# Kernel tuning notes

Measured on AMD Instinct MI355X. Metric: run time of the kernel, lower is better.

The kernel has to match this reference:

```python
import jax, jax.numpy as jnp
import numpy as np

B = 32768
L = 1024            # harmonics length (from 1365 = L + L//3)
HID = 256
OUT = 1024


def setup_inputs() -> dict:
    key = jax.random.key(0)
    k1, k2, k3 = jax.random.split(key, 3)
    x = jax.random.normal(k1, (B, 1, L), dtype=jnp.float32)
    W1 = jax.random.normal(k2, (HID, 1365), dtype=jnp.float32) * 0.02
    b1 = jnp.zeros((HID,), dtype=jnp.float32)
    W2 = jax.random.normal(k3, (OUT, HID), dtype=jnp.float32) * 0.02
    b2 = jnp.zeros((OUT,), dtype=jnp.float32)
    return {"x": x, "W1": W1, "b1": b1, "W2": W2, "b2": b2}


def reference(x, W1, b1, W2, b2):
    # backbone is identity; squeeze channel dim -> harmonics_pred [B, L]
    h = x[:, 0, :]
    # multi-scale average pooling (method='average'), vectorized over batch
    s1 = h                                               # scale 1: [B, 1024]
    s2 = h[:, : (L // 2) * 2].reshape(-1, L // 2, 2).mean(axis=-1)   # [B, 512]
    s3 = h[:, : (L // 3) * 3].reshape(-1, L // 3, 3).mean(axis=-1)   # [B, 341]
    m = L // 3                                           # min_len = 341
    summed = s1[:, :m] + s2[:, :m] + s3                  # [B, 341]
    feat = jnp.concatenate([h, summed], axis=1)          # [B, 1365]
    # fund_head MLP (dropout inactive in eval)
    hid = jax.nn.relu(feat @ W1.T + b1)                  # [B, 256]
    fund = hid @ W2.T + b2                               # [B, 1024]
    return fund[:, None, :], h
```

## Files before the change

kernel.cpp:

```cpp
#include <hip/hip_runtime.h>
#include <stdint.h>
#include <stddef.h>

typedef __attribute__((ext_vector_type(8))) short short8;
typedef __attribute__((ext_vector_type(4))) float floatx4;

#define MFMA_BF16(A, B, C) __builtin_amdgcn_mfma_f32_16x16x32_bf16((A), (B), (C), 0, 0, 0)

static constexpr int NB   = 32768;
static constexpr int LV   = 1024;
static constexpr int HIDV = 256;
static constexpr int OUTV = 1024;
static constexpr size_t HOFF = (size_t)NB * OUTV;

__device__ __forceinline__ short f2bf(float f) {
  union { float f; uint32_t u; } c; c.f = f;
  uint32_t u = c.u;
  u += 0x7fffu + ((u >> 16) & 1u);
  return (short)(u >> 16);
}

__global__ __launch_bounds__(256) void wprep(const float* __restrict__ W1,
                                             const float* __restrict__ W2,
                                             short* __restrict__ w1bf,
                                             short* __restrict__ w2bf) {
  int idx = blockIdx.x * 256 + threadIdx.x;
  if (idx < 256 * 1024) {
    int n = idx >> 10;
    int k = idx & 1023;
    const float* r = W1 + (size_t)n * 1365;
    float v = r[k];
    if (k < 341)  v += r[1024 + k];
    if (k < 682)  v += 0.5f * r[1024 + (k >> 1)];
    if (k < 1023) v += (1.f / 3.f) * r[1024 + k / 3];
    w1bf[idx] = f2bf(v);
  } else {
    int j = idx - 256 * 1024;
    w2bf[j] = f2bf(W2[j]);
  }
}

__global__ __launch_bounds__(512, 4) void gemm_fused(
    const float* __restrict__ x,
    const short* __restrict__ w1bf, const short* __restrict__ w2bf,
    const float* __restrict__ b1, const float* __restrict__ b2,
    float* __restrict__ out) {
  __shared__ __align__(16) short Abuf[2][64 * 72];
  __shared__ __align__(16) short Hbuf[64 * 264];

  const int tid  = threadIdx.x;
  const int wave = tid >> 6;
  const int lane = tid & 63;
  const int l15  = lane & 15;
  const int quad = lane >> 4;
  const int row0 = blockIdx.x * 64;

  const int srow = tid >> 3;
  const int sseg = tid & 7;

  float4 xa, xb;
  const floatx4 fzero = {0.f, 0.f, 0.f, 0.f};

  const float4* xrow = reinterpret_cast<const float4*>(x + (size_t)(row0 + srow) * LV);
  float4* hrow = reinterpret_cast<float4*>(out + HOFF + (size_t)(row0 + srow) * LV);

  auto loadA = [&](int ck) {
    xa = xrow[ck * 16 + 2 * sseg];
    xb = xrow[ck * 16 + 2 * sseg + 1];
  };
  auto writeA = [&](int buf) {
    short8 p;
    p[0] = f2bf(xa.x); p[1] = f2bf(xa.y); p[2] = f2bf(xa.z); p[3] = f2bf(xa.w);
    p[4] = f2bf(xb.x); p[5] = f2bf(xb.y); p[6] = f2bf(xb.z); p[7] = f2bf(xb.w);
    *reinterpret_cast<short8*>(&Abuf[buf][srow * 72 + sseg * 8]) = p;
  };
  auto storeH = [&](int ck) {
    hrow[ck * 16 + 2 * sseg]     = xa;
    hrow[ck * 16 + 2 * sseg + 1] = xb;
  };

  short8 Breg[4], Bnxt[4];
  auto loadB1 = [&](int ck, short8* dst) {
    #pragma unroll
    for (int ks = 0; ks < 2; ++ks)
      #pragma unroll
      for (int ns = 0; ns < 2; ++ns)
        dst[ks * 2 + ns] = *reinterpret_cast<const short8*>(
            w1bf + (size_t)(wave * 32 + ns * 16 + l15) * LV + ck * 64 + ks * 32 + quad * 8);
  };

  floatx4 acc1[4][2];
  #pragma unroll
  for (int ms = 0; ms < 4; ++ms)
    #pragma unroll
    for (int ns = 0; ns < 2; ++ns)
      acc1[ms][ns] = fzero;

  loadA(0);
  loadB1(0, Breg);

  #pragma unroll 1
  for (int ck = 0; ck < 16; ++ck) {
    const int buf = ck & 1;
    writeA(buf);
    asm volatile("s_waitcnt lgkmcnt(0)" ::: "memory");
    __builtin_amdgcn_s_barrier();
    asm volatile("" ::: "memory");
    storeH(ck);
    if (ck < 15) { loadA(ck + 1); loadB1(ck + 1, Bnxt); }
    #pragma unroll
    for (int ks = 0; ks < 2; ++ks) {
      short8 afr[4];
      #pragma unroll
      for (int ms = 0; ms < 4; ++ms)
        afr[ms] = *reinterpret_cast<const short8*>(
            &Abuf[buf][(ms * 16 + l15) * 72 + ks * 32 + quad * 8]);
      #pragma unroll
      for (int ms = 0; ms < 4; ++ms)
        #pragma unroll
        for (int ns = 0; ns < 2; ++ns)
          acc1[ms][ns] = MFMA_BF16(afr[ms], Breg[ks * 2 + ns], acc1[ms][ns]);
    }
    #pragma unroll
    for (int i = 0; i < 4; ++i) Breg[i] = Bnxt[i];
  }

  #pragma unroll
  for (int ms = 0; ms < 4; ++ms) {
    #pragma unroll
    for (int ns = 0; ns < 2; ++ns) {
      const int n = wave * 32 + ns * 16 + l15;
      const float bias = b1[n];
      #pragma unroll
      for (int r = 0; r < 4; ++r) {
        const int m = ms * 16 + quad * 4 + r;
        float v = acc1[ms][ns][r] + bias;
        Hbuf[m * 264 + n] = f2bf(v > 0.f ? v : 0.f);
      }
    }
  }
  asm volatile("s_waitcnt lgkmcnt(0)" ::: "memory");
  __builtin_amdgcn_s_barrier();
  asm volatile("" ::: "memory");

  short8 B2[2], B2n[2];
  auto loadB2 = [&](int q, int kc, short8* dst) {
    #pragma unroll
    for (int ns = 0; ns < 2; ++ns)
      dst[ns] = *reinterpret_cast<const short8*>(
          w2bf + (size_t)(q * 256 + wave * 32 + ns * 16 + l15) * HIDV + kc * 32 + quad * 8);
  };

  loadB2(0, 0, B2);
  #pragma unroll 1
  for (int q = 0; q < 4; ++q) {
    floatx4 acc2[4][2];
    #pragma unroll
    for (int ms = 0; ms < 4; ++ms)
      #pragma unroll
      for (int ns = 0; ns < 2; ++ns)
        acc2[ms][ns] = fzero;
    #pragma unroll 1
    for (int kc = 0; kc < 8; ++kc) {
      short8 afr[4];
      #pragma unroll
      for (int ms = 0; ms < 4; ++ms)
        afr[ms] = *reinterpret_cast<const short8*>(
            &Hbuf[(ms * 16 + l15) * 264 + kc * 32 + quad * 8]);
      const int t = q * 8 + kc + 1;
      if (t < 32) loadB2(t >> 3, t & 7, B2n);
      #pragma unroll
      for (int ms = 0; ms < 4; ++ms)
        #pragma unroll
        for (int ns = 0; ns < 2; ++ns)
          acc2[ms][ns] = MFMA_BF16(afr[ms], B2[ns], acc2[ms][ns]);
      #pragma unroll
      for (int i = 0; i < 2; ++i) B2[i] = B2n[i];
    }
    #pragma unroll
    for (int ms = 0; ms < 4; ++ms) {
      #pragma unroll
      for (int ns = 0; ns < 2; ++ns) {
        const int o = q * 256 + wave * 32 + ns * 16 + l15;
        const float bias = b2[o];
        #pragma unroll
        for (int r = 0; r < 4; ++r) {
          const int m = ms * 16 + quad * 4 + r;
          out[(size_t)(row0 + m) * OUTV + o] = acc2[ms][ns][r] + bias;
        }
      }
    }
  }
}

extern "C" void kernel_launch(void* const* d_in, const int* in_sizes, int n_in,
                              void* d_out, int out_size, void* d_ws, size_t ws_size,
                              hipStream_t stream) {
  const float* x  = (const float*)d_in[0];
  const float* W1 = (const float*)d_in[1];
  const float* b1 = (const float*)d_in[2];
  const float* W2 = (const float*)d_in[3];
  const float* b2 = (const float*)d_in[4];
  float* out = (float*)d_out;

  char* ws = (char*)d_ws;
  short* w1bf = (short*)(ws);
  short* w2bf = (short*)(ws + 524288);

  hipLaunchKernelGGL(wprep, dim3(2048), dim3(256), 0, stream, W1, W2, w1bf, w2bf);
  hipLaunchKernelGGL(gemm_fused, dim3(NB / 64), dim3(512), 0, stream,
                     x, w1bf, w2bf, b1, b2, out);
}
```

Baseline: 416.2 us.

## Prefetch x two chunks ahead and use nontemporal loads and stores

The A-tile load of x now runs two K-chunks ahead instead of one, using two register sets and a loop unrolled by two, so more global load latency is hidden behind the MFMA work. Loads of x, copies of h, and final output writes use nontemporal builtins, so streaming data bypasses and does not pollute the caches that hold the bf16 weights. The extra prefetch raises register pressure, which could hurt occupancy at the launch bound of 4 blocks.

```diff
diff --git a/kernel.cpp b/kernel.cpp
--- a/kernel.cpp
+++ b/kernel.cpp
@@ -58,25 +58,26 @@
   const int srow = tid >> 3;
   const int sseg = tid & 7;
 
-  float4 xa, xb;
   const floatx4 fzero = {0.f, 0.f, 0.f, 0.f};
 
-  const float4* xrow = reinterpret_cast<const float4*>(x + (size_t)(row0 + srow) * LV);
-  float4* hrow = reinterpret_cast<float4*>(out + HOFF + (size_t)(row0 + srow) * LV);
-
-  auto loadA = [&](int ck) {
-    xa = xrow[ck * 16 + 2 * sseg];
-    xb = xrow[ck * 16 + 2 * sseg + 1];
-  };
-  auto writeA = [&](int buf) {
+  const floatx4* xrow = reinterpret_cast<const floatx4*>(x + (size_t)(row0 + srow) * LV);
+  floatx4* hrow = reinterpret_cast<floatx4*>(out + HOFF + (size_t)(row0 + srow) * LV);
+
+  floatx4 xa0, xb0, xa1, xb1;
+
+  auto loadA = [&](int ck, floatx4& a, floatx4& b) {
+    a = __builtin_nontemporal_load(xrow + ck * 16 + 2 * sseg);
+    b = __builtin_nontemporal_load(xrow + ck * 16 + 2 * sseg + 1);
+  };
+  auto writeA = [&](int buf, const floatx4& a, const floatx4& b) {
     short8 p;
-    p[0] = f2bf(xa.x); p[1] = f2bf(xa.y); p[2] = f2bf(xa.z); p[3] = f2bf(xa.w);
-    p[4] = f2bf(xb.x); p[5] = f2bf(xb.y); p[6] = f2bf(xb.z); p[7] = f2bf(xb.w);
+    p[0] = f2bf(a[0]); p[1] = f2bf(a[1]); p[2] = f2bf(a[2]); p[3] = f2bf(a[3]);
+    p[4] = f2bf(b[0]); p[5] = f2bf(b[1]); p[6] = f2bf(b[2]); p[7] = f2bf(b[3]);
     *reinterpret_cast<short8*>(&Abuf[buf][srow * 72 + sseg * 8]) = p;
   };
-  auto storeH = [&](int ck) {
-    hrow[ck * 16 + 2 * sseg]     = xa;
-    hrow[ck * 16 + 2 * sseg + 1] = xb;
+  auto storeH = [&](int ck, const floatx4& a, const floatx4& b) {
+    __builtin_nontemporal_store(a, hrow + ck * 16 + 2 * sseg);
+    __builtin_nontemporal_store(b, hrow + ck * 16 + 2 * sseg + 1);
   };
 
   short8 Breg[4], Bnxt[4];
@@ -96,18 +97,18 @@
     for (int ns = 0; ns < 2; ++ns)
       acc1[ms][ns] = fzero;
 
-  loadA(0);
+  loadA(0, xa0, xb0);
+  loadA(1, xa1, xb1);
   loadB1(0, Breg);
 
-  #pragma unroll 1
-  for (int ck = 0; ck < 16; ++ck) {
-    const int buf = ck & 1;
-    writeA(buf);
+  auto kstep = [&](int ck, int buf, floatx4& a, floatx4& b) {
+    writeA(buf, a, b);
     asm volatile("s_waitcnt lgkmcnt(0)" ::: "memory");
     __builtin_amdgcn_s_barrier();
     asm volatile("" ::: "memory");
-    storeH(ck);
-    if (ck < 15) { loadA(ck + 1); loadB1(ck + 1, Bnxt); }
+    if (ck + 1 < 16) loadB1(ck + 1, Bnxt);
+    storeH(ck, a, b);
+    if (ck + 2 < 16) loadA(ck + 2, a, b);
     #pragma unroll
     for (int ks = 0; ks < 2; ++ks) {
       short8 afr[4];
@@ -123,6 +124,12 @@
     }
     #pragma unroll
     for (int i = 0; i < 4; ++i) Breg[i] = Bnxt[i];
+  };
+
+  #pragma unroll 1
+  for (int ck2 = 0; ck2 < 16; ck2 += 2) {
+    kstep(ck2,     0, xa0, xb0);
+    kstep(ck2 + 1, 1, xa1, xb1);
   }
 
   #pragma unroll
@@ -186,7 +193,8 @@
         #pragma unroll
         for (int r = 0; r < 4; ++r) {
           const int m = ms * 16 + quad * 4 + r;
-          out[(size_t)(row0 + m) * OUTV + o] = acc2[ms][ns][r] + bias;
+          __builtin_nontemporal_store(acc2[ms][ns][r] + bias,
+                                      &out[(size_t)(row0 + m) * OUTV + o]);
         }
       }
     }
```

New measurement: 418.1 us, median of 2. Within noise of the previous version (+0.5%).
